# Kernel tuning notes

Measured on AMD Instinct MI355X. Metric: run time of the kernel, lower is better.

## Reference

```python
import jax, jax.numpy as jnp
import numpy as np

EMBED_DIM = 256
UNITS = 512


def setup_inputs() -> dict:
    key = jax.random.key(0)
    ks = jax.random.split(key, 8)
    B, L = 2048, 64  # batch, 8*8 spatial locations
    features = jax.random.normal(ks[0], (B, L, EMBED_DIM), dtype=jnp.float32)
    hidden = jax.random.normal(ks[1], (B, UNITS), dtype=jnp.float32)
    s1 = 1.0 / np.sqrt(EMBED_DIM)
    s2 = 1.0 / np.sqrt(UNITS)
    W1 = jax.random.normal(ks[2], (EMBED_DIM, UNITS), dtype=jnp.float32) * s1
    b1 = jnp.zeros((UNITS,), dtype=jnp.float32)
    W2 = jax.random.normal(ks[3], (UNITS, UNITS), dtype=jnp.float32) * s2
    b2 = jnp.zeros((UNITS,), dtype=jnp.float32)
    V = jax.random.normal(ks[4], (UNITS, 1), dtype=jnp.float32) * s2
    bv = jnp.zeros((1,), dtype=jnp.float32)
    return {"features": features, "hidden": hidden, "W1": W1, "b1": b1,
            "W2": W2, "b2": b2, "V": V, "bv": bv}


def reference(features, hidden, W1, b1, W2, b2, V, bv):
    # features: [B, L, E], hidden: [B, U]
    # Bahdanau additive attention
    proj_f = jnp.einsum('ble,eu->blu', features, W1) + b1          # [B, L, U]
    proj_h = (hidden @ W2 + b2)[:, None, :]                        # [B, 1, U]
    e = jnp.tanh(proj_f + proj_h)                                  # [B, L, U]
    score = jnp.einsum('blu,uo->blo', e, V) + bv                   # [B, L, 1]
    attention_weights = jax.nn.softmax(score, axis=1)              # [B, L, 1]
    context_vector = jnp.sum(attention_weights * features, axis=1) # [B, E]
    return context_vector, attention_weights
```

## Files before the change

kernel.cpp:

```cpp
#include <hip/hip_runtime.h>
#include <math.h>

#define BATCH 2048
#define LDIM 64
#define EDIM 256
#define UDIM 512

typedef __attribute__((ext_vector_type(8))) _Float16 half8;
typedef __attribute__((ext_vector_type(4))) float floatx4;

__device__ inline float tanh_fast(float x) {
    float t = __builtin_amdgcn_exp2f(x * 2.88539008177792681f);
    return 1.f - 2.f * __builtin_amdgcn_rcpf(t + 1.f);
}
__device__ inline half8 cvt8(float4 f0, float4 f1) {
    half8 h;
    h[0] = (_Float16)f0.x; h[1] = (_Float16)f0.y;
    h[2] = (_Float16)f0.z; h[3] = (_Float16)f0.w;
    h[4] = (_Float16)f1.x; h[5] = (_Float16)f1.y;
    h[6] = (_Float16)f1.z; h[7] = (_Float16)f1.w;
    return h;
}
__device__ inline const half8* bfrag(const unsigned short* F, int kc, int ntg, int l) {
    return (const half8*)(F + ((((size_t)kc * 32 + ntg) * 64 + l) << 3));
}

__global__ __launch_bounds__(256) void prep_frag(const float* __restrict__ W1,
                                                 const float* __restrict__ W2,
                                                 unsigned short* __restrict__ F1,
                                                 unsigned short* __restrict__ F2) {
    __shared__ float S[32 * 128];
    int bid = blockIdx.x;
    const float* W; unsigned short* F; int kc, grp;
    if (bid < 32) { W = W1; F = F1; kc = bid >> 2; grp = bid & 3; }
    else { bid -= 32; W = W2; F = F2; kc = bid >> 2; grp = bid & 3; }
    const int tid = threadIdx.x;
    const float* src = W + (size_t)kc * 32 * UDIM + grp * 128;
    float4* Sv = (float4*)S;
#pragma unroll
    for (int i = 0; i < 4; ++i) {
        int f = tid + i * 256;
        int k = f >> 5, c4 = f & 31;
        Sv[f] = *(const float4*)(src + (size_t)k * UDIM + c4 * 4);
    }
    __syncthreads();
#pragma unroll
    for (int i = 0; i < 2; ++i) {
        int u = tid + i * 256;
        int lane = u & 63, ntl = u >> 6;
        int n_loc = ntl * 16 + (lane & 15);
        int k0 = (lane >> 4) * 8;
        half8 h;
#pragma unroll
        for (int j = 0; j < 8; ++j)
            h[j] = (_Float16)S[(k0 + j) * 128 + n_loc];
        int ntg = grp * 8 + ntl;
        *(half8*)(F + (((size_t)kc * 32 + ntg) * 64 + lane) * 8) = h;
    }
}

__global__ __launch_bounds__(256) void prep_ph(const float* __restrict__ hidden,
                                               const unsigned short* __restrict__ F2,
                                               const float* __restrict__ b1,
                                               const float* __restrict__ b2,
                                               float* __restrict__ ph) {
    const int tid = threadIdx.x;
    const int w = tid >> 6;
    const int l = tid & 63;
    const int r0 = blockIdx.x * 16;

    floatx4 acc[8];
#pragma unroll
    for (int i = 0; i < 8; ++i) acc[i] = (floatx4){0.f, 0.f, 0.f, 0.f};

    const float* ap = hidden + (size_t)(r0 + (l & 15)) * UDIM + ((l >> 4) << 3);

    float4 a0 = *(const float4*)(ap);
    float4 a1 = *(const float4*)(ap + 4);
    half8 B[8];
#pragma unroll
    for (int nt = 0; nt < 8; ++nt) B[nt] = *bfrag(F2, 0, w * 8 + nt, l);

    for (int kc = 0; kc < 16; ++kc) {
        half8 a = cvt8(a0, a1);
        float4 n0, n1; half8 NB[8];
        if (kc < 15) {
            n0 = *(const float4*)(ap + (kc + 1) * 32);
            n1 = *(const float4*)(ap + (kc + 1) * 32 + 4);
#pragma unroll
            for (int nt = 0; nt < 8; ++nt) NB[nt] = *bfrag(F2, kc + 1, w * 8 + nt, l);
        }
#pragma unroll
        for (int nt = 0; nt < 8; ++nt)
            acc[nt] = __builtin_amdgcn_mfma_f32_16x16x32_f16(a, B[nt], acc[nt], 0, 0, 0);
        if (kc < 15) {
            a0 = n0; a1 = n1;
#pragma unroll
            for (int nt = 0; nt < 8; ++nt) B[nt] = NB[nt];
        }
    }
#pragma unroll
    for (int nt = 0; nt < 8; ++nt) {
        const int n = (w * 8 + nt) * 16 + (l & 15);
        const float bias = b1[n] + b2[n];
#pragma unroll
        for (int r = 0; r < 4; ++r) {
            const int m = (l >> 4) * 4 + r;
            ph[(size_t)(r0 + m) * UDIM + n] = acc[nt][r] + bias;
        }
    }
}

__global__ __launch_bounds__(256, 2) void attn_main(
    const float* __restrict__ feat, const unsigned short* __restrict__ F1,
    const float* __restrict__ ph, const float* __restrict__ Vw,
    const float* __restrict__ bv,
    float* __restrict__ ctx_out, float* __restrict__ w_out)
{
    __shared__ unsigned short lA[2][4 * 64 * 8];
    __shared__ float phl[512];
    __shared__ float Vl[512];
    __shared__ float scp[4][64];
    __shared__ float wsm[64];

    const int tid = threadIdx.x;
    const int w = tid >> 6;
    const int l = tid & 63;
    const size_t b = blockIdx.x;
    const float* fb = feat + b * (LDIM * EDIM);

    ((float2*)phl)[tid] = ((const float2*)(ph + b * UDIM))[tid];
    ((float2*)Vl)[tid]  = ((const float2*)Vw)[tid];

    const int arow = tid >> 2, aoct = tid & 3;
    const float* aSrc = fb + arow * EDIM + aoct * 8;
    const int aidx = (((arow >> 4) * 64) + (aoct << 4) + (arow & 15)) * 8;

    floatx4 acc[8][4];
#pragma unroll
    for (int i = 0; i < 8; ++i)
#pragma unroll
        for (int j = 0; j < 4; ++j) acc[i][j] = (floatx4){0.f, 0.f, 0.f, 0.f};

    half8 Bc[8];
#pragma unroll
    for (int nt = 0; nt < 8; ++nt) Bc[nt] = *bfrag(F1, 0, w * 8 + nt, l);
    {
        float4 f0 = *(const float4*)(aSrc);
        float4 f1 = *(const float4*)(aSrc + 4);
        *(half8*)&lA[0][aidx] = cvt8(f0, f1);
    }
    __syncthreads();

#pragma unroll
    for (int kc = 0; kc < 8; ++kc) {
        const int cur = kc & 1;
        float4 n0, n1; half8 Bn[8];
        if (kc < 7) {
            n0 = *(const float4*)(aSrc + (kc + 1) * 32);
            n1 = *(const float4*)(aSrc + (kc + 1) * 32 + 4);
#pragma unroll
            for (int nt = 0; nt < 8; ++nt) Bn[nt] = *bfrag(F1, kc + 1, w * 8 + nt, l);
        }
        half8 a[4];
#pragma unroll
        for (int mt = 0; mt < 4; ++mt)
            a[mt] = *(const half8*)&lA[cur][(mt * 64 + l) * 8];
#pragma unroll
        for (int nt = 0; nt < 8; ++nt)
#pragma unroll
            for (int mt = 0; mt < 4; ++mt)
                acc[nt][mt] = __builtin_amdgcn_mfma_f32_16x16x32_f16(
                    a[mt], Bc[nt], acc[nt][mt], 0, 0, 0);
        if (kc < 7) {
            *(half8*)&lA[cur ^ 1][aidx] = cvt8(n0, n1);
#pragma unroll
            for (int nt = 0; nt < 8; ++nt) Bc[nt] = Bn[nt];
        }
        __syncthreads();
    }

    float sv[4][4];
#pragma unroll
    for (int mt = 0; mt < 4; ++mt)
#pragma unroll
        for (int r = 0; r < 4; ++r) sv[mt][r] = 0.f;
#pragma unroll
    for (int nt = 0; nt < 8; ++nt) {
        const int n = (w * 8 + nt) * 16 + (l & 15);
        const float phn = phl[n];
        const float vn  = Vl[n];
#pragma unroll
        for (int mt = 0; mt < 4; ++mt)
#pragma unroll
            for (int r = 0; r < 4; ++r)
                sv[mt][r] += tanh_fast(acc[nt][mt][r] + phn) * vn;
    }
#pragma unroll
    for (int mt = 0; mt < 4; ++mt)
#pragma unroll
        for (int r = 0; r < 4; ++r) {
            float v = sv[mt][r];
            v += __shfl_xor(v, 1);
            v += __shfl_xor(v, 2);
            v += __shfl_xor(v, 4);
            v += __shfl_xor(v, 8);
            if ((l & 15) == 0) scp[w][mt * 16 + (l >> 4) * 4 + r] = v;
        }
    __syncthreads();

    if (tid < 64) {
        float s = scp[0][tid] + scp[1][tid] + scp[2][tid] + scp[3][tid] + bv[0];
        float m = s;
        m = fmaxf(m, __shfl_xor(m, 32));
        m = fmaxf(m, __shfl_xor(m, 16));
        m = fmaxf(m, __shfl_xor(m, 8));
        m = fmaxf(m, __shfl_xor(m, 4));
        m = fmaxf(m, __shfl_xor(m, 2));
        m = fmaxf(m, __shfl_xor(m, 1));
        float e = __builtin_amdgcn_exp2f((s - m) * 1.44269504088896341f);
        float sum = e;
        sum += __shfl_xor(sum, 32);
        sum += __shfl_xor(sum, 16);
        sum += __shfl_xor(sum, 8);
        sum += __shfl_xor(sum, 4);
        sum += __shfl_xor(sum, 2);
        sum += __shfl_xor(sum, 1);
        float wgt = e / sum;
        wsm[tid] = wgt;
        w_out[b * LDIM + tid] = wgt;
    }
    __syncthreads();

    {
        float c = 0.f;
#pragma unroll 8
        for (int ll = 0; ll < LDIM; ++ll)
            c = fmaf(wsm[ll], fb[ll * EDIM + tid], c);
        ctx_out[b * EDIM + tid] = c;
    }
}

extern "C" void kernel_launch(void* const* d_in, const int* in_sizes, int n_in,
                              void* d_out, int out_size, void* d_ws, size_t ws_size,
                              hipStream_t stream) {
    const float* features = (const float*)d_in[0];
    const float* hidden   = (const float*)d_in[1];
    const float* W1       = (const float*)d_in[2];
    const float* b1       = (const float*)d_in[3];
    const float* W2       = (const float*)d_in[4];
    const float* b2       = (const float*)d_in[5];
    const float* Vw       = (const float*)d_in[6];
    const float* bv       = (const float*)d_in[7];

    float* ctx_out = (float*)d_out;
    float* w_out   = (float*)d_out + (size_t)BATCH * EDIM;

    float* ph = (float*)d_ws;
    unsigned short* F1 = (unsigned short*)(ph + (size_t)BATCH * UDIM);
    unsigned short* F2 = F1 + (size_t)8 * 32 * 64 * 8;

    prep_frag<<<dim3(96), dim3(256), 0, stream>>>(W1, W2, F1, F2);
    prep_ph<<<dim3(128), dim3(256), 0, stream>>>(hidden, F2, b1, b2, ph);
    attn_main<<<dim3(BATCH), dim3(256), 0, stream>>>(
        features, F1, ph, Vw, bv, ctx_out, w_out);
}
```

Before: 261.3 us.

## Use 512-thread blocks and stage the full feature tile in swizzled LDS

The main attention kernel now runs 8 waves per batch row instead of 4, with each wave owning 4 N-tiles rather than 8, which halves the accumulator registers per thread. The whole 64x256 feature tile is loaded and converted to fp16 into LDS once, using an XOR swizzle. This replaces the double-buffered K-loop and its per-iteration barriers. The context reduction is split across two halves of the L dimension and combined through shared memory. The intent is higher occupancy and fewer synchronisations, at the cost of more LDS per block and no overlap of global loads with the MFMA work.

```diff
diff --git a/kernel.cpp b/kernel.cpp
--- a/kernel.cpp
+++ b/kernel.cpp
@@ -111,17 +111,18 @@
     }
 }
 
-__global__ __launch_bounds__(256, 2) void attn_main(
+__global__ __launch_bounds__(512, 4) void attn_main(
     const float* __restrict__ feat, const unsigned short* __restrict__ F1,
     const float* __restrict__ ph, const float* __restrict__ Vw,
     const float* __restrict__ bv,
     float* __restrict__ ctx_out, float* __restrict__ w_out)
 {
-    __shared__ unsigned short lA[2][4 * 64 * 8];
+    __shared__ unsigned short lA[8 * 4 * 64 * 8];
     __shared__ float phl[512];
     __shared__ float Vl[512];
-    __shared__ float scp[4][64];
+    __shared__ float scp[8][64];
     __shared__ float wsm[64];
+    __shared__ float ctxp[2][256];
 
     const int tid = threadIdx.x;
     const int w = tid >> 6;
@@ -129,55 +130,48 @@
     const size_t b = blockIdx.x;
     const float* fb = feat + b * (LDIM * EDIM);
 
-    ((float2*)phl)[tid] = ((const float2*)(ph + b * UDIM))[tid];
-    ((float2*)Vl)[tid]  = ((const float2*)Vw)[tid];
-
-    const int arow = tid >> 2, aoct = tid & 3;
-    const float* aSrc = fb + arow * EDIM + aoct * 8;
-    const int aidx = (((arow >> 4) * 64) + (aoct << 4) + (arow & 15)) * 8;
-
-    floatx4 acc[8][4];
-#pragma unroll
-    for (int i = 0; i < 8; ++i)
+    float4 f4[2][4];
+#pragma unroll
+    for (int p = 0; p < 2; ++p) {
+        const int u = tid + 512 * p;
+        const float4* gp = (const float4*)(fb + (u >> 4) * EDIM + (u & 15) * 16);
+        f4[p][0] = gp[0]; f4[p][1] = gp[1]; f4[p][2] = gp[2]; f4[p][3] = gp[3];
+    }
+    phl[tid] = ph[b * UDIM + tid];
+    Vl[tid]  = Vw[tid];
+
+#pragma unroll
+    for (int p = 0; p < 2; ++p) {
+        const int u  = tid + 512 * p;
+        const int r  = u >> 4, kc = (u & 15) >> 1, o = (u & 1) * 2;
+        const int mt = r >> 4, rr = r & 15;
+        const int base = (kc * 4 + mt) * 64;
+        *(half8*)&lA[(base + ((o * 16 + rr) ^ kc)) * 8]       = cvt8(f4[p][0], f4[p][1]);
+        *(half8*)&lA[(base + (((o + 1) * 16 + rr) ^ kc)) * 8] = cvt8(f4[p][2], f4[p][3]);
+    }
+
+    floatx4 acc[4][4];
+#pragma unroll
+    for (int i = 0; i < 4; ++i)
 #pragma unroll
         for (int j = 0; j < 4; ++j) acc[i][j] = (floatx4){0.f, 0.f, 0.f, 0.f};
 
-    half8 Bc[8];
-#pragma unroll
-    for (int nt = 0; nt < 8; ++nt) Bc[nt] = *bfrag(F1, 0, w * 8 + nt, l);
-    {
-        float4 f0 = *(const float4*)(aSrc);
-        float4 f1 = *(const float4*)(aSrc + 4);
-        *(half8*)&lA[0][aidx] = cvt8(f0, f1);
-    }
-    __syncthreads();
-
-#pragma unroll
+    __syncthreads();
+
     for (int kc = 0; kc < 8; ++kc) {
-        const int cur = kc & 1;
-        float4 n0, n1; half8 Bn[8];
-        if (kc < 7) {
-            n0 = *(const float4*)(aSrc + (kc + 1) * 32);
-            n1 = *(const float4*)(aSrc + (kc + 1) * 32 + 4);
-#pragma unroll
-            for (int nt = 0; nt < 8; ++nt) Bn[nt] = *bfrag(F1, kc + 1, w * 8 + nt, l);
-        }
+        half8 Bc[4];
+#pragma unroll
+        for (int nt = 0; nt < 4; ++nt) Bc[nt] = *bfrag(F1, kc, w * 4 + nt, l);
         half8 a[4];
 #pragma unroll
         for (int mt = 0; mt < 4; ++mt)
-            a[mt] = *(const half8*)&lA[cur][(mt * 64 + l) * 8];
-#pragma unroll
-        for (int nt = 0; nt < 8; ++nt)
+            a[mt] = *(const half8*)&lA[((kc * 4 + mt) * 64 + (l ^ kc)) * 8];
+#pragma unroll
+        for (int nt = 0; nt < 4; ++nt)
 #pragma unroll
             for (int mt = 0; mt < 4; ++mt)
                 acc[nt][mt] = __builtin_amdgcn_mfma_f32_16x16x32_f16(
                     a[mt], Bc[nt], acc[nt][mt], 0, 0, 0);
-        if (kc < 7) {
-            *(half8*)&lA[cur ^ 1][aidx] = cvt8(n0, n1);
-#pragma unroll
-            for (int nt = 0; nt < 8; ++nt) Bc[nt] = Bn[nt];
-        }
-        __syncthreads();
     }
 
     float sv[4][4];
@@ -186,8 +180,8 @@
 #pragma unroll
         for (int r = 0; r < 4; ++r) sv[mt][r] = 0.f;
 #pragma unroll
-    for (int nt = 0; nt < 8; ++nt) {
-        const int n = (w * 8 + nt) * 16 + (l & 15);
+    for (int nt = 0; nt < 4; ++nt) {
+        const int n = (w * 4 + nt) * 16 + (l & 15);
         const float phn = phl[n];
         const float vn  = Vl[n];
 #pragma unroll
@@ -210,7 +204,9 @@
     __syncthreads();
 
     if (tid < 64) {
-        float s = scp[0][tid] + scp[1][tid] + scp[2][tid] + scp[3][tid] + bv[0];
+        float s = bv[0];
+#pragma unroll
+        for (int wv = 0; wv < 8; ++wv) s += scp[wv][tid];
         float m = s;
         m = fmaxf(m, __shfl_xor(m, 32));
         m = fmaxf(m, __shfl_xor(m, 16));
@@ -233,12 +229,16 @@
     __syncthreads();
 
     {
+        const int e = tid & 255, h = tid >> 8;
         float c = 0.f;
 #pragma unroll 8
-        for (int ll = 0; ll < LDIM; ++ll)
-            c = fmaf(wsm[ll], fb[ll * EDIM + tid], c);
-        ctx_out[b * EDIM + tid] = c;
-    }
+        for (int ll = h * 32; ll < h * 32 + 32; ++ll)
+            c = fmaf(wsm[ll], fb[ll * EDIM + e], c);
+        ctxp[h][e] = c;
+    }
+    __syncthreads();
+    if (tid < 256)
+        ctx_out[b * EDIM + tid] = ctxp[0][tid] + ctxp[1][tid];
 }
 
 extern "C" void kernel_launch(void* const* d_in, const int* in_sizes, int n_in,
@@ -262,6 +262,6 @@
 
     prep_frag<<<dim3(96), dim3(256), 0, stream>>>(W1, W2, F1, F2);
     prep_ph<<<dim3(128), dim3(256), 0, stream>>>(hidden, F2, b1, b2, ph);
-    attn_main<<<dim3(BATCH), dim3(256), 0, stream>>>(
+    attn_main<<<dim3(BATCH), dim3(512), 0, stream>>>(
         features, F1, ph, Vw, bv, ctx_out, w_out);
 }
```

Result: no change. 257.5 us (-1.5%).
